# Optimization experiments

Measured on AMD Instinct MI355X. Metric: run time of the kernel, lower is better.

## Reference

```python
import jax, jax.numpy as jnp
import numpy as np

EMB = 128
N_LIG = 32768
N_REC = 262144
NUM_GRAPHS = 1024
E_LIG = 327680
E_REC = 2097152
LIG_DIMS = [119, 9, 11, 12, 9, 5, 8, 2, 2]
NUM_LAYERS = 3
BN_EPS = 1e-5


def setup_inputs() -> dict:
    key = jax.random.key(0)
    ks = iter(jax.random.split(key, 64))

    lig_x = jnp.stack(
        [jax.random.randint(next(ks), (N_LIG,), 0, d) for d in LIG_DIMS], axis=1
    )  # [N_lig, 9] categorical atom features
    atom_offsets = jnp.asarray(np.cumsum([0] + LIG_DIMS[:-1]), dtype=jnp.int32)
    atom_emb = jax.random.normal(next(ks), (sum(LIG_DIMS), EMB), jnp.float32) * 0.1

    rec_x_int = jax.random.randint(next(ks), (N_REC,), 0, 20)
    rec_x_float = jax.random.normal(next(ks), (N_REC, 199), jnp.float32)
    rec_emb1 = jax.random.normal(next(ks), (20, EMB), jnp.float32) * 0.1
    rec_w = jax.random.normal(next(ks), (199, EMB), jnp.float32) * 0.05
    rec_b = jnp.zeros((EMB,), jnp.float32)

    lig_edge_index = jax.random.randint(next(ks), (2, E_LIG), 0, N_LIG)
    rec_edge_index = jax.random.randint(next(ks), (2, E_REC), 0, N_REC)
    lig_batch = jnp.repeat(jnp.arange(NUM_GRAPHS), N_LIG // NUM_GRAPHS)
    rec_batch = jnp.repeat(jnp.arange(NUM_GRAPHS), N_REC // NUM_GRAPHS)

    def layer_params():
        W = jax.random.normal(next(ks), (NUM_LAYERS, EMB, EMB), jnp.float32) * (1.0 / np.sqrt(EMB))
        b = jnp.zeros((NUM_LAYERS, EMB), jnp.float32)
        gamma = jnp.ones((NUM_LAYERS, EMB), jnp.float32)
        beta = jnp.zeros((NUM_LAYERS, EMB), jnp.float32)
        return W, b, gamma, beta

    lig_W, lig_b, lig_gamma, lig_beta = layer_params()
    rec_W, rec_bc, rec_gamma, rec_beta = layer_params()

    out_w1 = jax.random.normal(next(ks), (2 * EMB, EMB), jnp.float32) * (1.0 / np.sqrt(2 * EMB))
    out_b1 = jnp.zeros((EMB,), jnp.float32)
    out_w2 = jax.random.normal(next(ks), (EMB, 1), jnp.float32) * (1.0 / np.sqrt(EMB))
    out_b2 = jnp.zeros((1,), jnp.float32)

    return dict(
        lig_x=lig_x, rec_x_int=rec_x_int, rec_x_float=rec_x_float,
        lig_edge_index=lig_edge_index, rec_edge_index=rec_edge_index,
        lig_batch=lig_batch, rec_batch=rec_batch, atom_offsets=atom_offsets,
        atom_emb=atom_emb, rec_emb1=rec_emb1, rec_w=rec_w, rec_b=rec_b,
        lig_W=lig_W, lig_b=lig_b, lig_gamma=lig_gamma, lig_beta=lig_beta,
        rec_W=rec_W, rec_bc=rec_bc, rec_gamma=rec_gamma, rec_beta=rec_beta,
        out_w1=out_w1, out_b1=out_b1, out_w2=out_w2, out_b2=out_b2,
    )


def gcn_layer(x, edge_index, W, b, gamma, beta):
    """GCNConv (sym-norm, self loops) -> BatchNorm (batch stats) -> ReLU."""
    n = x.shape[0]
    h = x @ W  # [N, EMB]
    loops = jnp.arange(n)
    src = jnp.concatenate([edge_index[0], loops])
    dst = jnp.concatenate([edge_index[1], loops])
    deg = jax.ops.segment_sum(jnp.ones_like(dst, dtype=h.dtype), dst, num_segments=n)
    dinv = jax.lax.rsqrt(jnp.maximum(deg, 1.0))  # deg >= 1 with self loops
    msg = h[src] * (dinv[src] * dinv[dst])[:, None]  # gather + normalize
    out = jax.ops.segment_sum(msg, dst, num_segments=n) + b
    mu = out.mean(axis=0)
    var = out.var(axis=0)
    out = (out - mu) * jax.lax.rsqrt(var + BN_EPS) * gamma + beta
    return jax.nn.relu(out)


def scatter_mean(x, seg, num_segments):
    s = jax.ops.segment_sum(x, seg, num_segments=num_segments)
    cnt = jax.ops.segment_sum(jnp.ones((x.shape[0],), x.dtype), seg, num_segments=num_segments)
    return s / jnp.maximum(cnt, 1.0)[:, None]


def reference(lig_x, rec_x_int, rec_x_float, lig_edge_index, rec_edge_index,
              lig_batch, rec_batch, atom_offsets, atom_emb, rec_emb1, rec_w, rec_b,
              lig_W, lig_b, lig_gamma, lig_beta, rec_W, rec_bc, rec_gamma, rec_beta,
              out_w1, out_b1, out_w2, out_b2):
    # Node encoders
    lig_h = atom_emb[lig_x + atom_offsets[None, :]].sum(axis=1)        # [N_lig, EMB]
    rec_h = rec_emb1[rec_x_int] + rec_x_float @ rec_w + rec_b          # [N_rec, EMB]

    for l in range(NUM_LAYERS):
        lig_h = gcn_layer(lig_h, lig_edge_index, lig_W[l], lig_b[l], lig_gamma[l], lig_beta[l])
        rec_h = gcn_layer(rec_h, rec_edge_index, rec_W[l], rec_bc[l], rec_gamma[l], rec_beta[l])

    lig_feat = scatter_mean(lig_h, lig_batch, NUM_GRAPHS)
    rec_feat = scatter_mean(rec_h, rec_batch, NUM_GRAPHS)
    z = jnp.concatenate([lig_feat, rec_feat], axis=1)                  # [B, 2*EMB]
    z = jax.nn.relu(z @ out_w1 + out_b1)
    return (z @ out_w2 + out_b2).squeeze(-1)                            # [B]
```

## Files before the change

kernel.cpp:

```cpp
#include <hip/hip_runtime.h>
#include <hip/hip_bf16.h>
#include <cstdint>
#include <cstddef>

#define EMB 128
#define NLIG 32768
#define NREC 262144
#define NGRAPH 1024
#define ELIG 327680
#define EREC 2097152
#define BN_EPS 1e-5f

typedef unsigned short ushort_t;
typedef short bf16x8 __attribute__((ext_vector_type(8)));
typedef float f32x4 __attribute__((ext_vector_type(4)));

__device__ __forceinline__ float bf2f(ushort_t u) {
  union { unsigned int i; float f; } v;
  v.i = ((unsigned int)u) << 16;
  return v.f;
}
__device__ __forceinline__ ushort_t f2bf(float f) {
  __hip_bfloat16 h = __float2bfloat16(f);
  union { __hip_bfloat16 h; ushort_t u; } v;
  v.h = h;
  return v.u;
}


__global__ __launch_bounds__(256)
void gk_count(const int* __restrict__ dst, int* __restrict__ cnt, int E) {
  int e = blockIdx.x * 256 + threadIdx.x;
  if (e < E) atomicAdd(&cnt[dst[e]], 1);
}

__global__ __launch_bounds__(256)
void gk_scan1(const int* __restrict__ cnt, int* __restrict__ off,
              int* __restrict__ bsum, int n) {
  __shared__ int sm[256];
  int t = threadIdx.x;
  int base = blockIdx.x * 1024 + t * 4;
  int v0 = (base + 0 < n) ? cnt[base + 0] : 0;
  int v1 = (base + 1 < n) ? cnt[base + 1] : 0;
  int v2 = (base + 2 < n) ? cnt[base + 2] : 0;
  int v3 = (base + 3 < n) ? cnt[base + 3] : 0;
  int loc = v0 + v1 + v2 + v3;
  sm[t] = loc;
  __syncthreads();
  for (int o = 1; o < 256; o <<= 1) {
    int x = (t >= o) ? sm[t - o] : 0;
    __syncthreads();
    sm[t] += x;
    __syncthreads();
  }
  int run = sm[t] - loc;
  if (base + 0 < n) off[base + 0] = run;
  run += v0;
  if (base + 1 < n) off[base + 1] = run;
  run += v1;
  if (base + 2 < n) off[base + 2] = run;
  run += v2;
  if (base + 3 < n) off[base + 3] = run;
  if (t == 255) bsum[blockIdx.x] = sm[255];
}

__global__ __launch_bounds__(256)
void gk_scan2(int* __restrict__ bsum, int nb) {
  __shared__ int sm[256];
  int t = threadIdx.x;
  int v = (t < nb) ? bsum[t] : 0;
  sm[t] = v;
  __syncthreads();
  for (int o = 1; o < 256; o <<= 1) {
    int x = (t >= o) ? sm[t - o] : 0;
    __syncthreads();
    sm[t] += x;
    __syncthreads();
  }
  if (t < nb) bsum[t] = sm[t] - v;
}

__global__ __launch_bounds__(256)
void gk_scan3(int* __restrict__ off, const int* __restrict__ bsum, int n, int E) {
  int i = blockIdx.x * 256 + threadIdx.x;
  if (i < n) off[i] += bsum[i >> 10];
  if (i == 0) off[n] = E;
}

__global__ __launch_bounds__(256)
void gk_copy(int* __restrict__ d, const int* __restrict__ s, int n) {
  int i = blockIdx.x * 256 + threadIdx.x;
  if (i < n) d[i] = s[i];
}

__global__ __launch_bounds__(256)
void gk_fill(const int* __restrict__ src, const int* __restrict__ dst,
             int* __restrict__ cur, int* __restrict__ csr, int E) {
  int e = blockIdx.x * 256 + threadIdx.x;
  if (e < E) {
    int d = dst[e];
    int pos = atomicAdd(&cur[d], 1);
    csr[pos] = src[e];
  }
}

__global__ __launch_bounds__(256)
void gk_dinv(const int* __restrict__ off, float* __restrict__ dinv, int n) {
  int i = blockIdx.x * 256 + threadIdx.x;
  if (i < n) dinv[i] = rsqrtf((float)(off[i + 1] - off[i] + 1));
}


__global__ __launch_bounds__(128)
void gk_ligenc(const int* __restrict__ lig_x, const int* __restrict__ offs,
               const float* __restrict__ emb, ushort_t* __restrict__ A) {
  __shared__ int idx[9];
  int i = blockIdx.x;
  int c = threadIdx.x;
  if (c < 9) idx[c] = lig_x[i * 9 + c] + offs[c];
  __syncthreads();
  float acc = 0.f;
#pragma unroll
  for (int f = 0; f < 9; ++f) acc += emb[(size_t)idx[f] * EMB + c];
  A[(size_t)i * EMB + c] = f2bf(acc);
}

__global__ __launch_bounds__(256)
void gk_recw(const float* __restrict__ W, ushort_t* __restrict__ Wt) {
  int idx = blockIdx.x * 256 + threadIdx.x;
  int c = idx >> 8, k = idx & 255;
  Wt[(size_t)c * 256 + k] = (k < 199) ? f2bf(W[(size_t)k * 128 + c]) : (ushort_t)0;
}

__global__ __launch_bounds__(256)
void gk_recenc(const float* __restrict__ X, const int* __restrict__ xi,
               const float* __restrict__ emb1, const ushort_t* __restrict__ Wt,
               const float* __restrict__ b, ushort_t* __restrict__ A) {
  __shared__ ushort_t Ws[128 * 256];
  __shared__ ushort_t Xs[128 * 40];
  const int K = 199;
  int t = threadIdx.x;
  int row0 = blockIdx.x * 128;
  int w = t >> 6, lane = t & 63;
  int m = lane & 15, quad = lane >> 4;
  int rbase = w * 32;

  for (int u = t; u < 4096; u += 256) {
    int c = u >> 5, cc = u & 31;
    uint4 v = *(const uint4*)(Wt + (size_t)c * 256 + cc * 8);
    *(uint4*)&Ws[c * 256 + ((cc ^ (c & 15)) * 8)] = v;
  }

  f32x4 acc[2][8];
#pragma unroll
  for (int rt = 0; rt < 2; ++rt)
#pragma unroll
    for (int ct = 0; ct < 8; ++ct) acc[rt][ct] = (f32x4){0.f, 0.f, 0.f, 0.f};

  for (int ch = 0; ch < 7; ++ch) {
    int kc = ch * 32;
    __syncthreads();
    for (int u = t; u < 512; u += 256) {
      int r = u >> 2, sub = u & 3;
      const float* xr = X + (size_t)(row0 + r) * K + kc + sub * 8;
      ushort_t tmp[8];
#pragma unroll
      for (int j = 0; j < 8; ++j) {
        int k = kc + sub * 8 + j;
        float v = (k < K) ? xr[j] : 0.f;
        tmp[j] = f2bf(v);
      }
      *(uint4*)&Xs[r * 40 + sub * 8] = *(uint4*)tmp;
    }
    __syncthreads();

    bf16x8 a0 = *(const bf16x8*)&Xs[(rbase + m) * 40 + quad * 8];
    bf16x8 a1 = *(const bf16x8*)&Xs[(rbase + 16 + m) * 40 + quad * 8];
    int L = ch * 4 + quad;
#pragma unroll
    for (int ct = 0; ct < 8; ++ct) {
      bf16x8 bb = *(const bf16x8*)&Ws[(ct * 16 + m) * 256 + ((L ^ m) * 8)];
      acc[0][ct] = __builtin_amdgcn_mfma_f32_16x16x32_bf16(a0, bb, acc[0][ct], 0, 0, 0);
      acc[1][ct] = __builtin_amdgcn_mfma_f32_16x16x32_bf16(a1, bb, acc[1][ct], 0, 0, 0);
    }
  }

  float bcol[8];
#pragma unroll
  for (int ct = 0; ct < 8; ++ct) bcol[ct] = b[ct * 16 + m];
#pragma unroll
  for (int rt = 0; rt < 2; ++rt) {
    int rb = row0 + rbase + rt * 16 + quad * 4;
#pragma unroll
    for (int rr = 0; rr < 4; ++rr) {
      int row = rb + rr;
      const float* e = emb1 + (size_t)xi[row] * 128;
#pragma unroll
      for (int ct = 0; ct < 8; ++ct) {
        int c = ct * 16 + m;
        float v = acc[rt][ct][rr] + bcol[ct] + e[c];
        A[(size_t)row * 128 + c] = f2bf(v);
      }
    }
  }
}

__global__ __launch_bounds__(256)
void gk_prep(const float* __restrict__ W, const float* __restrict__ stats,
             const float* __restrict__ gamma, const float* __restrict__ beta,
             float inv_n, int donorm, ushort_t* __restrict__ Wt,
             float* __restrict__ bnscl, float* __restrict__ bnsh) {
  int idx = blockIdx.x * 256 + threadIdx.x;
  if (idx < 128) {
    if (donorm) {
      float mu = stats[idx] * inv_n;
      float var = stats[128 + idx] * inv_n - mu * mu;
      float s = gamma[idx] * rsqrtf(var + BN_EPS);
      bnscl[idx] = s;
      bnsh[idx] = beta[idx] - mu * s;
    } else {
      bnscl[idx] = 1.f;
      bnsh[idx] = 0.f;
    }
  }
  int c = idx >> 7, k = idx & 127;
  Wt[(size_t)c * 128 + k] = f2bf(W[(size_t)k * 128 + c]);
}

__global__ __launch_bounds__(256)
void gk_mm(const ushort_t* __restrict__ Xb, const ushort_t* __restrict__ Wt,
           const float* __restrict__ bnscl, const float* __restrict__ bnsh,
           int donorm, const float* __restrict__ dinv,
           ushort_t* __restrict__ gb) {
  __shared__ ushort_t Xs[128 * 128];
  __shared__ ushort_t Ws[128 * 128];
  int t = threadIdx.x;
  int row0 = blockIdx.x * 128;

  for (int i = t; i < 2048; i += 256) {
    int r = i >> 4, cc = i & 15;
    union { uint4 v; ushort_t s[8]; } u;
    u.v = *(const uint4*)(Xb + (size_t)(row0 + r) * 128 + cc * 8);
    if (donorm) {
#pragma unroll
      for (int j = 0; j < 8; ++j) {
        int k = cc * 8 + j;
        float f = fmaf(bf2f(u.s[j]), bnscl[k], bnsh[k]);
        f = f > 0.f ? f : 0.f;
        u.s[j] = f2bf(f);
      }
    }
    *(uint4*)&Xs[r * 128 + ((cc ^ (r & 15)) * 8)] = u.v;
  }
  for (int i = t; i < 2048; i += 256) {
    int c = i >> 4, cc = i & 15;
    uint4 u = *(const uint4*)(Wt + (size_t)c * 128 + cc * 8);
    *(uint4*)&Ws[c * 128 + ((cc ^ (c & 15)) * 8)] = u;
  }
  __syncthreads();

  int w = t >> 6, lane = t & 63;
  int m = lane & 15, quad = lane >> 4;
  int rbase = w * 32;

  f32x4 acc[2][8];
#pragma unroll
  for (int rt = 0; rt < 2; ++rt)
#pragma unroll
    for (int ct = 0; ct < 8; ++ct) acc[rt][ct] = (f32x4){0.f, 0.f, 0.f, 0.f};

#pragma unroll
  for (int kc8 = 0; kc8 < 16; kc8 += 4) {
    int ck = (kc8 + quad) ^ m;
    bf16x8 a0 = *(const bf16x8*)&Xs[(rbase + m) * 128 + ck * 8];
    bf16x8 a1 = *(const bf16x8*)&Xs[(rbase + 16 + m) * 128 + ck * 8];
#pragma unroll
    for (int ct = 0; ct < 8; ++ct) {
      bf16x8 b = *(const bf16x8*)&Ws[(ct * 16 + m) * 128 + ck * 8];
      acc[0][ct] = __builtin_amdgcn_mfma_f32_16x16x32_bf16(a0, b, acc[0][ct], 0, 0, 0);
      acc[1][ct] = __builtin_amdgcn_mfma_f32_16x16x32_bf16(a1, b, acc[1][ct], 0, 0, 0);
    }
  }

#pragma unroll
  for (int rt = 0; rt < 2; ++rt) {
    int rb = row0 + rbase + rt * 16 + quad * 4;
    float d0 = dinv[rb + 0], d1 = dinv[rb + 1];
    float d2 = dinv[rb + 2], d3 = dinv[rb + 3];
#pragma unroll
    for (int ct = 0; ct < 8; ++ct) {
      int c = ct * 16 + m;
      gb[(size_t)(rb + 0) * 128 + c] = f2bf(acc[rt][ct][0] * d0);
      gb[(size_t)(rb + 1) * 128 + c] = f2bf(acc[rt][ct][1] * d1);
      gb[(size_t)(rb + 2) * 128 + c] = f2bf(acc[rt][ct][2] * d2);
      gb[(size_t)(rb + 3) * 128 + c] = f2bf(acc[rt][ct][3] * d3);
    }
  }
}


struct Quad {
  int i0, i1, i2, i3;
  float m0, m1, m2, m3;
};

__device__ __forceinline__ Quad load_quad(const int* __restrict__ csr,
                                          int e, int e1, int safe) {
  Quad q;
  int c0 = (e + 0 < e1) ? e + 0 : safe;
  int c1 = (e + 1 < e1) ? e + 1 : safe;
  int c2 = (e + 2 < e1) ? e + 2 : safe;
  int c3 = (e + 3 < e1) ? e + 3 : safe;
  q.i0 = csr[c0];
  q.i1 = csr[c1];
  q.i2 = csr[c2];
  q.i3 = csr[c3];
  q.m0 = (e + 0 < e1) ? 1.f : 0.f;
  q.m1 = (e + 1 < e1) ? 1.f : 0.f;
  q.m2 = (e + 2 < e1) ? 1.f : 0.f;
  q.m3 = (e + 3 < e1) ? 1.f : 0.f;
  return q;
}

__device__ __forceinline__ void gather4(const ushort_t* __restrict__ g, int c0,
                                        const Quad& q, unsigned int* v) {
  v[0] = *(const unsigned int*)(g + (size_t)q.i0 * 128 + c0);
  v[1] = *(const unsigned int*)(g + (size_t)q.i1 * 128 + c0);
  v[2] = *(const unsigned int*)(g + (size_t)q.i2 * 128 + c0);
  v[3] = *(const unsigned int*)(g + (size_t)q.i3 * 128 + c0);
}

__device__ __forceinline__ void consume4(float2& acc, const Quad& q,
                                         const unsigned int* v) {
  float lo0 = bf2f((ushort_t)(v[0] & 0xffffu)), hi0 = bf2f((ushort_t)(v[0] >> 16));
  float lo1 = bf2f((ushort_t)(v[1] & 0xffffu)), hi1 = bf2f((ushort_t)(v[1] >> 16));
  float lo2 = bf2f((ushort_t)(v[2] & 0xffffu)), hi2 = bf2f((ushort_t)(v[2] >> 16));
  float lo3 = bf2f((ushort_t)(v[3] & 0xffffu)), hi3 = bf2f((ushort_t)(v[3] >> 16));
  acc.x = fmaf(lo0, q.m0, acc.x); acc.y = fmaf(hi0, q.m0, acc.y);
  acc.x = fmaf(lo1, q.m1, acc.x); acc.y = fmaf(hi1, q.m1, acc.y);
  acc.x = fmaf(lo2, q.m2, acc.x); acc.y = fmaf(hi2, q.m2, acc.y);
  acc.x = fmaf(lo3, q.m3, acc.x); acc.y = fmaf(hi3, q.m3, acc.y);
}

__global__ __launch_bounds__(256)
void gk_agg(const ushort_t* __restrict__ g, const int* __restrict__ off,
            const int* __restrict__ csr, const float* __restrict__ dinv,
            ushort_t* __restrict__ outb, float* __restrict__ stats) {
  __shared__ float ls[128];
  __shared__ float lss[128];
  int t = threadIdx.x;
  int slot = t >> 6;
  int lane = t & 63;
  int c0 = lane * 2;
  int i0 = blockIdx.x * 32;

  if (t < 128) { ls[t] = 0.f; lss[t] = 0.f; }
  __syncthreads();

  float sx = 0.f, sy = 0.f, ssx = 0.f, ssy = 0.f;

  for (int p = 0; p < 4; ++p) {
    int rA = i0 + slot * 2 + p * 8;
    int rB = rA + 1;
    int eA = off[rA], eA1 = off[rA + 1];
    int eB1 = off[rB + 1];
    int eB = eA1;
    float dA = dinv[rA], dB = dinv[rB];
    unsigned int uA = *(const unsigned int*)(g + (size_t)rA * 128 + c0);
    unsigned int uB = *(const unsigned int*)(g + (size_t)rB * 128 + c0);
    float2 accA = make_float2(bf2f((ushort_t)(uA & 0xffffu)),
                              bf2f((ushort_t)(uA >> 16)));
    float2 accB = make_float2(bf2f((ushort_t)(uB & 0xffffu)),
                              bf2f((ushort_t)(uB >> 16)));
    int safeA = (eA1 > eA) ? eA1 - 1 : 0;
    int safeB = (eB1 > eB) ? eB1 - 1 : 0;

    Quad qA = load_quad(csr, eA, eA1, safeA);
    Quad qB = load_quad(csr, eB, eB1, safeB);
    unsigned int vA[4], vB[4];
    gather4(g, c0, qA, vA);
    gather4(g, c0, qB, vB);
    int e_A = eA + 4, e_B = eB + 4;

    while (e_A < eA1 || e_B < eB1) {
      bool an = e_A < eA1;
      bool bn = e_B < eB1;
      Quad qA2, qB2;
      unsigned int wA[4], wB[4];
      if (an) {
        qA2 = load_quad(csr, e_A, eA1, safeA);
        gather4(g, c0, qA2, wA);
      }
      if (bn) {
        qB2 = load_quad(csr, e_B, eB1, safeB);
        gather4(g, c0, qB2, wB);
      }
      consume4(accA, qA, vA);
      consume4(accB, qB, vB);
      if (an) {
        qA = qA2; vA[0] = wA[0]; vA[1] = wA[1]; vA[2] = wA[2]; vA[3] = wA[3];
        e_A += 4;
      } else {
        qA.m0 = qA.m1 = qA.m2 = qA.m3 = 0.f;
      }
      if (bn) {
        qB = qB2; vB[0] = wB[0]; vB[1] = wB[1]; vB[2] = wB[2]; vB[3] = wB[3];
        e_B += 4;
      } else {
        qB.m0 = qB.m1 = qB.m2 = qB.m3 = 0.f;
      }
    }
    consume4(accA, qA, vA);
    consume4(accB, qB, vB);

    accA.x *= dA; accA.y *= dA;
    accB.x *= dB; accB.y *= dB;
    unsigned int oA = (unsigned int)f2bf(accA.x) | ((unsigned int)f2bf(accA.y) << 16);
    unsigned int oB = (unsigned int)f2bf(accB.x) | ((unsigned int)f2bf(accB.y) << 16);
    *(unsigned int*)(outb + (size_t)rA * 128 + c0) = oA;
    *(unsigned int*)(outb + (size_t)rB * 128 + c0) = oB;
    sx += accA.x + accB.x;
    sy += accA.y + accB.y;
    ssx = fmaf(accA.x, accA.x, ssx); ssx = fmaf(accB.x, accB.x, ssx);
    ssy = fmaf(accA.y, accA.y, ssy); ssy = fmaf(accB.y, accB.y, ssy);
  }

  atomicAdd(&ls[c0 + 0], sx);
  atomicAdd(&ls[c0 + 1], sy);
  atomicAdd(&lss[c0 + 0], ssx);
  atomicAdd(&lss[c0 + 1], ssy);
  __syncthreads();
  if (t < 128) {
    atomicAdd(&stats[t], ls[t]);
    atomicAdd(&stats[t + 128], lss[t]);
  }
}

__global__ __launch_bounds__(128)
void gk_pool(const ushort_t* __restrict__ A, const float* __restrict__ stats,
             const float* __restrict__ gamma, const float* __restrict__ beta,
             float inv_n, float* __restrict__ z, int npg, int zoff) {
  int gidx = blockIdx.x;
  int c = threadIdx.x;
  float mu = stats[c] * inv_n;
  float var = stats[128 + c] * inv_n - mu * mu;
  float scl = gamma[c] * rsqrtf(var + BN_EPS);
  float be = beta[c];
  float sum = 0.f;
  int r0 = gidx * npg;
  for (int r = 0; r < npg; ++r) {
    float v = (bf2f(A[(size_t)(r0 + r) * 128 + c]) - mu) * scl + be;
    sum += v > 0.f ? v : 0.f;
  }
  z[(size_t)gidx * 256 + zoff + c] = sum * (1.0f / (float)npg);
}

__global__ __launch_bounds__(128)
void gk_mlp(const float* __restrict__ z, const float* __restrict__ w1,
            const float* __restrict__ b1, const float* __restrict__ w2,
            const float* __restrict__ b2, float* __restrict__ out) {
  __shared__ float zs[256];
  __shared__ float red[128];
  int gidx = blockIdx.x, t = threadIdx.x;
  zs[t] = z[(size_t)gidx * 256 + t];
  zs[t + 128] = z[(size_t)gidx * 256 + 128 + t];
  __syncthreads();
  float acc = b1[t];
  for (int k = 0; k < 256; ++k) acc += zs[k] * w1[(size_t)k * 128 + t];
  acc = (acc > 0.f ? acc : 0.f) * w2[t];
  red[t] = acc;
  __syncthreads();
  for (int o = 64; o > 0; o >>= 1) {
    if (t < o) red[t] += red[t + o];
    __syncthreads();
  }
  if (t == 0) out[gidx] = red[0] + b2[0];
}


extern "C" void kernel_launch(void* const* d_in, const int* in_sizes, int n_in,
                              void* d_out, int out_size, void* d_ws, size_t ws_size,
                              hipStream_t stream) {
  (void)in_sizes; (void)n_in; (void)out_size; (void)ws_size;
  const int*   lig_x       = (const int*)  d_in[0];
  const int*   rec_x_int   = (const int*)  d_in[1];
  const float* rec_x_float = (const float*)d_in[2];
  const int*   lig_ei      = (const int*)  d_in[3];
  const int*   rec_ei      = (const int*)  d_in[4];
  const int*   atom_off    = (const int*)  d_in[7];
  const float* atom_emb    = (const float*)d_in[8];
  const float* rec_emb1    = (const float*)d_in[9];
  const float* rec_w       = (const float*)d_in[10];
  const float* rec_b       = (const float*)d_in[11];
  const float* lig_W       = (const float*)d_in[12];
  const float* lig_gamma   = (const float*)d_in[14];
  const float* lig_beta    = (const float*)d_in[15];
  const float* rec_W       = (const float*)d_in[16];
  const float* rec_gamma   = (const float*)d_in[18];
  const float* rec_beta    = (const float*)d_in[19];
  const float* out_w1      = (const float*)d_in[20];
  const float* out_b1      = (const float*)d_in[21];
  const float* out_w2      = (const float*)d_in[22];
  const float* out_b2      = (const float*)d_in[23];
  float* out = (float*)d_out;

  char* p = (char*)d_ws;
  auto alloc = [&](size_t bytes) -> void* {
    void* r = p;
    p += (bytes + 255) & ~(size_t)255;
    return r;
  };
  ushort_t* Ab     = (ushort_t*)alloc((size_t)NREC * EMB * 2);
  ushort_t* Gb     = (ushort_t*)alloc((size_t)NREC * EMB * 2);
  ushort_t* Wtb    = (ushort_t*)alloc((size_t)EMB * EMB * 2);
  ushort_t* Wt256  = (ushort_t*)alloc((size_t)EMB * 256 * 2);
  float* bnscl     = (float*)alloc(128 * 4);
  float* bnsh      = (float*)alloc(128 * 4);
  float* dinv_lig  = (float*)alloc((size_t)NLIG * 4);
  float* dinv_rec  = (float*)alloc((size_t)NREC * 4);
  int*   cnt_lig   = (int*)  alloc((size_t)NLIG * 4);
  int*   cnt_rec   = (int*)  alloc((size_t)NREC * 4);
  int*   off_lig   = (int*)  alloc((size_t)(NLIG + 1) * 4);
  int*   off_rec   = (int*)  alloc((size_t)(NREC + 1) * 4);
  int*   csr_lig   = (int*)  alloc((size_t)ELIG * 4);
  int*   csr_rec   = (int*)  alloc((size_t)EREC * 4);
  int*   bsum_lig  = (int*)  alloc(256 * 4);
  int*   bsum_rec  = (int*)  alloc(256 * 4);
  float* stats     = (float*)alloc(256 * 4);
  float* z         = (float*)alloc((size_t)NGRAPH * 256 * 4);

  hipMemsetAsync(cnt_lig, 0, (size_t)NLIG * 4, stream);
  hipMemsetAsync(cnt_rec, 0, (size_t)NREC * 4, stream);
  gk_count<<<ELIG / 256, 256, 0, stream>>>(lig_ei + ELIG, cnt_lig, ELIG);
  gk_count<<<EREC / 256, 256, 0, stream>>>(rec_ei + EREC, cnt_rec, EREC);
  gk_scan1<<<NLIG / 1024, 256, 0, stream>>>(cnt_lig, off_lig, bsum_lig, NLIG);
  gk_scan2<<<1, 256, 0, stream>>>(bsum_lig, NLIG / 1024);
  gk_scan3<<<NLIG / 256, 256, 0, stream>>>(off_lig, bsum_lig, NLIG, ELIG);
  gk_scan1<<<NREC / 1024, 256, 0, stream>>>(cnt_rec, off_rec, bsum_rec, NREC);
  gk_scan2<<<1, 256, 0, stream>>>(bsum_rec, NREC / 1024);
  gk_scan3<<<NREC / 256, 256, 0, stream>>>(off_rec, bsum_rec, NREC, EREC);
  gk_copy<<<NLIG / 256, 256, 0, stream>>>(cnt_lig, off_lig, NLIG);
  gk_copy<<<NREC / 256, 256, 0, stream>>>(cnt_rec, off_rec, NREC);
  gk_fill<<<ELIG / 256, 256, 0, stream>>>(lig_ei, lig_ei + ELIG, cnt_lig, csr_lig, ELIG);
  gk_fill<<<EREC / 256, 256, 0, stream>>>(rec_ei, rec_ei + EREC, cnt_rec, csr_rec, EREC);
  gk_dinv<<<NLIG / 256, 256, 0, stream>>>(off_lig, dinv_lig, NLIG);
  gk_dinv<<<NREC / 256, 256, 0, stream>>>(off_rec, dinv_rec, NREC);

  auto run_entity = [&](const float* Wall, const float* gamma, const float* beta,
                        const int* offv, const int* csrv, const float* dinv,
                        int n, int npg, int zoff) {
    float inv_n = 1.0f / (float)n;
    for (int l = 0; l < 3; ++l) {
      const float* W = Wall + (size_t)l * EMB * EMB;
      const float* gm = (l > 0) ? gamma + (size_t)(l - 1) * EMB : gamma;
      const float* bt = (l > 0) ? beta + (size_t)(l - 1) * EMB : beta;
      gk_prep<<<64, 256, 0, stream>>>(W, stats, gm, bt, inv_n, l > 0 ? 1 : 0,
                                      Wtb, bnscl, bnsh);
      hipMemsetAsync(stats, 0, 256 * 4, stream);
      gk_mm<<<n / 128, 256, 0, stream>>>(Ab, Wtb, bnscl, bnsh, l > 0 ? 1 : 0,
                                         dinv, Gb);
      gk_agg<<<n / 32, 256, 0, stream>>>(Gb, offv, csrv, dinv, Ab, stats);
    }
    gk_pool<<<NGRAPH, 128, 0, stream>>>(Ab, stats, gamma + 2 * EMB, beta + 2 * EMB,
                                        inv_n, z, npg, zoff);
  };

  gk_ligenc<<<NLIG, 128, 0, stream>>>(lig_x, atom_off, atom_emb, Ab);
  run_entity(lig_W, lig_gamma, lig_beta, off_lig, csr_lig, dinv_lig,
             NLIG, NLIG / NGRAPH, 0);

  gk_recw<<<128, 256, 0, stream>>>(rec_w, Wt256);
  gk_recenc<<<NREC / 128, 256, 0, stream>>>(rec_x_float, rec_x_int, rec_emb1,
                                            Wt256, rec_b, Ab);
  run_entity(rec_W, rec_gamma, rec_beta, off_rec, csr_rec, dinv_rec,
             NREC, NREC / NGRAPH, EMB);

  gk_mlp<<<NGRAPH, 128, 0, stream>>>(z, out_w1, out_b1, out_w2, out_b2, out);
}
```

Baseline: 1.899 ms.

## Pre-cast receptor features to bf16 and feed MFMA directly from global memory

Adds a separate grid-stride kernel that converts the fp32 receptor float features into a padded bf16 buffer with a 200-element row stride. The encoder GEMM then loads its A and B MFMA fragments straight from global memory, dropping the LDS staging and the per-chunk __syncthreads. The weight transpose is shrunk to a 224-wide K layout. This trades an extra write and read of the bf16 copy for a simpler, barrier-free inner loop. The last K chunk reads past the 200-element row into the next row or into the unzeroed tail padding, and relies on the zeroed weight columns to cancel those values.

```diff
diff --git a/kernel.cpp b/kernel.cpp
--- a/kernel.cpp
+++ b/kernel.cpp
@@ -126,30 +126,43 @@
 }
 
 __global__ __launch_bounds__(256)
-void gk_recw(const float* __restrict__ W, ushort_t* __restrict__ Wt) {
+void gk_recw2(const float* __restrict__ W, ushort_t* __restrict__ Wt) {
   int idx = blockIdx.x * 256 + threadIdx.x;
-  int c = idx >> 8, k = idx & 255;
-  Wt[(size_t)c * 256 + k] = (k < 199) ? f2bf(W[(size_t)k * 128 + c]) : (ushort_t)0;
-}
-
-__global__ __launch_bounds__(256)
-void gk_recenc(const float* __restrict__ X, const int* __restrict__ xi,
-               const float* __restrict__ emb1, const ushort_t* __restrict__ Wt,
-               const float* __restrict__ b, ushort_t* __restrict__ A) {
-  __shared__ ushort_t Ws[128 * 256];
-  __shared__ ushort_t Xs[128 * 40];
-  const int K = 199;
+  if (idx < 128 * 224) {
+    int c = idx / 224, k = idx - c * 224;
+    Wt[idx] = (k < 199) ? f2bf(W[(size_t)k * 128 + c]) : (ushort_t)0;
+  }
+}
+
+__global__ __launch_bounds__(256)
+void gk_xcast(const float* __restrict__ X, ushort_t* __restrict__ Xb) {
+  const int ITEMS = NREC * 25;
+  int stride = gridDim.x * 256;
+  for (int v = blockIdx.x * 256 + threadIdx.x; v < ITEMS; v += stride) {
+    int row = v / 25, sub = v - row * 25;
+    int k0 = sub * 8;
+    const float* xr = X + (size_t)row * 199 + k0;
+    ushort_t tmp[8];
+#pragma unroll
+    for (int j = 0; j < 8; ++j) {
+      float f = (k0 + j < 199) ? xr[j] : 0.f;
+      tmp[j] = f2bf(f);
+    }
+    *(uint4*)(Xb + (size_t)row * 200 + k0) = *(uint4*)tmp;
+  }
+}
+
+__global__ __launch_bounds__(256)
+void gk_recenc2(const ushort_t* __restrict__ Xb, const int* __restrict__ xi,
+                const float* __restrict__ emb1, const ushort_t* __restrict__ Wt,
+                const float* __restrict__ b, ushort_t* __restrict__ A) {
   int t = threadIdx.x;
   int row0 = blockIdx.x * 128;
   int w = t >> 6, lane = t & 63;
   int m = lane & 15, quad = lane >> 4;
   int rbase = w * 32;
-
-  for (int u = t; u < 4096; u += 256) {
-    int c = u >> 5, cc = u & 31;
-    uint4 v = *(const uint4*)(Wt + (size_t)c * 256 + cc * 8);
-    *(uint4*)&Ws[c * 256 + ((cc ^ (c & 15)) * 8)] = v;
-  }
+  int rA = row0 + rbase + m;
+  int rB = rA + 16;
 
   f32x4 acc[2][8];
 #pragma unroll
@@ -157,29 +170,16 @@
 #pragma unroll
     for (int ct = 0; ct < 8; ++ct) acc[rt][ct] = (f32x4){0.f, 0.f, 0.f, 0.f};
 
+  const ushort_t* xpA = Xb + (size_t)rA * 200 + quad * 8;
+  const ushort_t* xpB = Xb + (size_t)rB * 200 + quad * 8;
+  const ushort_t* wp = Wt + (size_t)m * 224 + quad * 8;
+
   for (int ch = 0; ch < 7; ++ch) {
-    int kc = ch * 32;
-    __syncthreads();
-    for (int u = t; u < 512; u += 256) {
-      int r = u >> 2, sub = u & 3;
-      const float* xr = X + (size_t)(row0 + r) * K + kc + sub * 8;
-      ushort_t tmp[8];
-#pragma unroll
-      for (int j = 0; j < 8; ++j) {
-        int k = kc + sub * 8 + j;
-        float v = (k < K) ? xr[j] : 0.f;
-        tmp[j] = f2bf(v);
-      }
-      *(uint4*)&Xs[r * 40 + sub * 8] = *(uint4*)tmp;
-    }
-    __syncthreads();
-
-    bf16x8 a0 = *(const bf16x8*)&Xs[(rbase + m) * 40 + quad * 8];
-    bf16x8 a1 = *(const bf16x8*)&Xs[(rbase + 16 + m) * 40 + quad * 8];
-    int L = ch * 4 + quad;
+    bf16x8 a0 = *(const bf16x8*)(xpA + ch * 32);
+    bf16x8 a1 = *(const bf16x8*)(xpB + ch * 32);
 #pragma unroll
     for (int ct = 0; ct < 8; ++ct) {
-      bf16x8 bb = *(const bf16x8*)&Ws[(ct * 16 + m) * 256 + ((L ^ m) * 8)];
+      bf16x8 bb = *(const bf16x8*)(wp + (size_t)ct * 16 * 224 + ch * 32);
       acc[0][ct] = __builtin_amdgcn_mfma_f32_16x16x32_bf16(a0, bb, acc[0][ct], 0, 0, 0);
       acc[1][ct] = __builtin_amdgcn_mfma_f32_16x16x32_bf16(a1, bb, acc[1][ct], 0, 0, 0);
     }
@@ -513,7 +513,8 @@
   ushort_t* Ab     = (ushort_t*)alloc((size_t)NREC * EMB * 2);
   ushort_t* Gb     = (ushort_t*)alloc((size_t)NREC * EMB * 2);
   ushort_t* Wtb    = (ushort_t*)alloc((size_t)EMB * EMB * 2);
-  ushort_t* Wt256  = (ushort_t*)alloc((size_t)EMB * 256 * 2);
+  ushort_t* WtK    = (ushort_t*)alloc((size_t)EMB * 224 * 2);
+  ushort_t* Xb2    = (ushort_t*)alloc(((size_t)NREC * 200 + 64) * 2);
   float* bnscl     = (float*)alloc(128 * 4);
   float* bnsh      = (float*)alloc(128 * 4);
   float* dinv_lig  = (float*)alloc((size_t)NLIG * 4);
@@ -569,9 +570,10 @@
   run_entity(lig_W, lig_gamma, lig_beta, off_lig, csr_lig, dinv_lig,
              NLIG, NLIG / NGRAPH, 0);
 
-  gk_recw<<<128, 256, 0, stream>>>(rec_w, Wt256);
-  gk_recenc<<<NREC / 128, 256, 0, stream>>>(rec_x_float, rec_x_int, rec_emb1,
-                                            Wt256, rec_b, Ab);
+  gk_recw2<<<112, 256, 0, stream>>>(rec_w, WtK);
+  gk_xcast<<<2048, 256, 0, stream>>>(rec_x_float, Xb2);
+  gk_recenc2<<<NREC / 128, 256, 0, stream>>>(Xb2, rec_x_int, rec_emb1,
+                                             WtK, rec_b, Ab);
   run_entity(rec_W, rec_gamma, rec_beta, off_rec, csr_rec, dinv_rec,
              NREC, NREC / NGRAPH, EMB);
 
```

After: 1.900 ms. About the same (+0.0%).
